# Kernel tuning notes

Measured on AMD Instinct MI355X. Metric: run time of the kernel, lower is better.

## Reference

```python
import jax, jax.numpy as jnp
import numpy as np

N_QUBITS = 10
N_LAYERS = 2
QSVT_DEGREE = 3
DT_RANK = 5  # n_qubits // 2
PI = np.float32(np.pi)

# ---- batched statevector simulation helpers (wire 0 = most significant, as in pennylane default.qubit) ----

def _apply_1q(s, wire, U):
    # s: (batch,) + (2,)*n complex; U: (batch,2,2) or (2,2)
    s = jnp.moveaxis(s, 1 + wire, 1)
    shp = s.shape
    s2 = s.reshape(shp[0], 2, -1)
    if U.ndim == 3:
        out = jnp.einsum('bij,bjr->bir', U, s2)
    else:
        out = jnp.einsum('ij,bjr->bir', U, s2)
    return jnp.moveaxis(out.reshape(shp), 1, 1 + wire)

def _ry(t):
    c = jnp.cos(t / 2).astype(jnp.complex64)
    s = jnp.sin(t / 2).astype(jnp.complex64)
    return jnp.stack([jnp.stack([c, -s], -1), jnp.stack([s, c], -1)], -2)

def _rz(t):
    e = jnp.exp(-0.5j * jnp.asarray(t).astype(jnp.complex64))
    z = jnp.zeros_like(e)
    return jnp.stack([jnp.stack([e, z], -1), jnp.stack([z, jnp.conj(e)], -1)], -2)

def _rx(t):
    c = jnp.cos(t / 2).astype(jnp.complex64)
    s = (-1j) * jnp.sin(t / 2).astype(jnp.complex64)
    return jnp.stack([jnp.stack([c, s], -1), jnp.stack([s, c], -1)], -2)

def _cnot(s, control, target):
    f = jnp.flip(s, axis=1 + target)
    s0 = jax.lax.index_in_dim(s, 0, axis=1 + control, keepdims=True)
    f1 = jax.lax.index_in_dim(f, 1, axis=1 + control, keepdims=True)
    return jnp.concatenate([s0, f1], axis=1 + control)

def _circuit(h, x, dt, cp, pc):
    """Batched selective QSVT circuit; h,x,dt: (B,n). Returns <Z_i> per wire, (B,n) float32."""
    n = N_QUBITS
    b = h.shape[0]
    s = jnp.zeros((b, 2 ** n), jnp.complex64).at[:, 0].set(1.0).reshape((b,) + (2,) * n)
    # 1. state encoding
    for i in range(n):
        s = _apply_1q(s, i, _ry(h[:, i]))
    # 2. delta-modulated QSVT block
    for d in range(QSVT_DEGREE + 1):
        for i in range(n):
            s = _apply_1q(s, i, _rz(pc[d] * dt[:, i] * PI))
        for i in range(n - 1):
            s = _cnot(s, i, i + 1)
        s = _cnot(s, n - 1, 0)
    # 3. variational block
    k = 0
    for _ in range(N_LAYERS):
        for i in range(n):
            s = _apply_1q(s, i, _rx(cp[k]))
            s = _apply_1q(s, i, _ry(cp[k + 1]))
            s = _apply_1q(s, i, _rz(cp[k + 2]))
            k += 3
        for i in range(n - 1):
            s = _cnot(s, i, i + 1)
    # 4. delta-modulated input encoding
    for i in range(n):
        s = _apply_1q(s, i, _ry(x[:, i] * dt[:, i]))
    # 5. <Z_i> measurements
    p = s.real ** 2 + s.imag ** 2
    zs = [(jax.lax.index_in_dim(p, 0, 1 + i, False) - jax.lax.index_in_dim(p, 1, 1 + i, False)).reshape(b, -1).sum(-1) for i in range(n)]
    return jnp.stack(zs, -1).astype(jnp.float32)

def setup_inputs() -> dict:
    key = jax.random.key(0)
    ks = jax.random.split(key, 6)
    B, S, n, r = 128, 512, N_QUBITS, DT_RANK
    angles = jax.random.uniform(ks[0], (B, S, n), jnp.float32) * PI  # angle encoding in [0, pi]
    W_x = jax.random.normal(ks[1], (r + 2 * n, n), jnp.float32) * 0.3  # x_proj weight (no bias)
    W_dt = jax.random.normal(ks[2], (n, r), jnp.float32) * 0.3  # dt_proj weight
    rng = np.random.default_rng(0)
    dt0 = np.exp(rng.random(n) * (np.log(0.1) - np.log(0.001)) + np.log(0.001))
    b_dt = jnp.asarray(dt0 + np.log(-np.expm1(-dt0)), jnp.float32)  # inverse-softplus init
    poly_coeffs = jax.random.normal(ks[3], (QSVT_DEGREE + 1,), jnp.float32) * 0.1
    circuit_params = jax.random.normal(ks[4], (n * N_LAYERS * 3,), jnp.float32) * 0.1
    D = jnp.ones((n,), jnp.float32)
    return {"angles": angles, "W_x": W_x, "W_dt": W_dt, "b_dt": b_dt,
            "poly_coeffs": poly_coeffs, "circuit_params": circuit_params, "D": D}

def reference(angles, W_x, W_dt, b_dt, poly_coeffs, circuit_params, D):
    # selective projections
    x_dbc = jnp.einsum('bsn,kn->bsk', angles, W_x)
    dt_raw = x_dbc[..., :DT_RANK]
    # B slice (x_dbc[..., DT_RANK:DT_RANK+n]) is computed but unused in the original forward
    C = x_dbc[..., DT_RANK + N_QUBITS:]
    dt = jax.nn.softplus(jnp.einsum('bsr,nr->bsn', dt_raw, W_dt) + b_dt)
    dt_angles = jnp.tanh(dt) * PI
    # quantum recurrence uses detached tensors in the original (torch .detach())
    x_sg = jax.lax.stop_gradient(angles)
    dt_sg = jax.lax.stop_gradient(dt_angles)
    cp = jax.lax.stop_gradient(circuit_params)
    pc = jax.lax.stop_gradient(poly_coeffs)

    def step(h, xs):
        x_t, d_t = xs
        h2 = _circuit(h, x_t, d_t, cp, pc)
        return h2, h2

    h0 = jnp.zeros((angles.shape[0], N_QUBITS), jnp.float32)
    _, hs = jax.lax.scan(step, h0, (jnp.swapaxes(x_sg, 0, 1), jnp.swapaxes(dt_sg, 0, 1)))
    hs = jnp.swapaxes(hs, 0, 1)  # (B,S,n)
    return C * hs + D * angles
```

## Files before the change

kernel.cpp:

```cpp
#include <hip/hip_runtime.h>
#include <math.h>


#define PIF 3.14159265358979323846f

constexpr int NQ = 10, SEQ = 512, NB = 128, NTHR = 512, RECF = 36;

struct CTbl { int mz[4][NQ]; };
constexpr CTbl build_tbl() {
  CTbl t{};
  unsigned mrow[NQ];
  for (int b = 0; b < NQ; ++b) mrow[b] = 1u << b;
  for (int d = 0; d < 4; ++d) {
    for (int i = 0; i < NQ; ++i) t.mz[d][i] = (int)mrow[9 - i];
    for (int i = 0; i < NQ - 1; ++i) { int bc = 9 - i, bt = 8 - i; mrow[bt] ^= mrow[bc]; }
    mrow[9] ^= mrow[0];
  }
  return t;
}
constexpr CTbl CT = build_tbl();

struct PermCols { int c4[10]; int cL[10]; };
constexpr PermCols build_perms() {
  PermCols P{};
  for (int b = 0; b < 10; ++b) {
    int x = 1 << b;
    for (int d = 0; d < 4; ++d) {
      for (int i = 0; i < 9; ++i) { int bc = 9 - i, bt = 8 - i; if ((x >> bc) & 1) x ^= (1 << bt); }
      if (x & 1) x ^= (1 << 9);
    }
    P.c4[b] = x;
    int y = 1 << b;
    for (int i = 0; i < 9; ++i) { int bc = 9 - i, bt = 8 - i; if ((y >> bc) & 1) y ^= (1 << bt); }
    P.cL[b] = y;
  }
  return P;
}
constexpr PermCols PC = build_perms();

constexpr int lanePart(int x)  { return ((x >> 0) & 1) | (((x >> 5) & 1) << 1) |
                                        (((x >> 1) & 1) << 2) | (((x >> 7) & 1) << 3) |
                                        (((x >> 3) & 1) << 4) | (((x >> 9) & 1) << 5); }
constexpr int wavePart8(int x) { return ((x >> 4) & 1) | (((x >> 8) & 1) << 1) |
                                        (((x >> 6) & 1) << 2); }

typedef __attribute__((ext_vector_type(2))) float v2;

constexpr int VOFS[8] = {0, 16, 256, 272, 64, 80, 320, 336};

template<int C>
__device__ __forceinline__ int dpp1(int x) {
  return __builtin_amdgcn_update_dpp(x, x, C, 0xF, 0xF, false);
}
template<int VL>
__device__ __forceinline__ int lxi(int x) {
  if constexpr (VL == 1)  return dpp1<0xB1>(x);
  else if constexpr (VL == 2)  return dpp1<0x4E>(x);
  else if constexpr (VL == 3)  return dpp1<0x1B>(x);
  else if constexpr (VL <= 7) {
    constexpr int q = (VL & 3) ^ 3;
    int y = x;
    if constexpr (q == 1) y = dpp1<0xB1>(y);
    else if constexpr (q == 2) y = dpp1<0x4E>(y);
    else if constexpr (q == 3) y = dpp1<0x1B>(y);
    return dpp1<0x141>(y);
  } else if constexpr (VL >= 12) {
    constexpr int q = (VL & 3) ^ 3;
    int y = x;
    if constexpr (q == 1) y = dpp1<0xB1>(y);
    else if constexpr (q == 2) y = dpp1<0x4E>(y);
    else if constexpr (q == 3) y = dpp1<0x1B>(y);
    return dpp1<0x140>(y);
  } else {
    constexpr int a = VL & 3;
    int y = x;
    if constexpr (a == 1) y = dpp1<0xB1>(y);
    else if constexpr (a == 2) y = dpp1<0x4E>(y);
    else if constexpr (a == 3) y = dpp1<0x1B>(y);
    y = dpp1<0x141>(y);
    return dpp1<0x140>(y);
  }
}
template<int VL>
__device__ __forceinline__ float lx(float x) {
  if constexpr (VL == 0) return x;
  else if constexpr (VL & 32) {
    int addr = (((int)threadIdx.x & 63) ^ VL) << 2;
    return __int_as_float(__builtin_amdgcn_ds_bpermute(addr, __float_as_int(x)));
  } else if constexpr (VL & 16) {
    return __int_as_float(__builtin_amdgcn_ds_swizzle(__float_as_int(x), (VL << 10) | 0x1F));
  } else {
    return __int_as_float(lxi<VL>(__float_as_int(x)));
  }
}
__device__ __forceinline__ float rdl(float x, int l) {
  return __int_as_float(__builtin_amdgcn_readlane(__float_as_int(x), l));
}

__device__ __forceinline__ int swz(int j) {
  return j ^ (((j >> 5) & 1) << 2) ^ ((j >> 7) & 1);
}

__device__ __forceinline__ void apply2(v2* amp, const v2* p, bool par, float4 U0, float4 U1) {
  v2 u00 = {U0.x, U0.y}, u01 = {U0.z, U0.w}, u10 = {U1.x, U1.y}, u11 = {U1.z, U1.w};
  v2 A = par ? u11 : u00, B = par ? u10 : u01;
  v2 An = {-A.y, A.y}, Bn = {-B.y, B.y};
#pragma unroll
  for (int r = 0; r < 2; ++r) {
    v2 o = amp[r], q = p[r];
    v2 res = A.x * o;
    res += An * __builtin_shufflevector(o, o, 1, 0);
    res += B.x * q;
    res += Bn * __builtin_shufflevector(q, q, 1, 0);
    amp[r] = res;
  }
}

template<int VL>
__device__ __forceinline__ void gate_lane2(v2* amp, float4 U0, float4 U1, int lane) {
  v2 p[2];
#pragma unroll
  for (int r = 0; r < 2; ++r) { p[r].x = lx<VL>(amp[r].x); p[r].y = lx<VL>(amp[r].y); }
  apply2(amp, p, (lane & VL) != 0, U0, U1);
}

__device__ __forceinline__ void gate_reg1(v2* amp, float4 U0, float4 U1) {
  v2 u00 = {U0.x, U0.y}, u01 = {U0.z, U0.w}, u10 = {U1.x, U1.y}, u11 = {U1.z, U1.w};
  v2 o0 = amp[0], o1 = amp[1];
  v2 a0 = {0.f, 0.f}, a1 = {0.f, 0.f};
  a0.x += u00.x * o0.x - u00.y * o0.y;  a0.y += u00.x * o0.y + u00.y * o0.x;
  a0.x += u01.x * o1.x - u01.y * o1.y;  a0.y += u01.x * o1.y + u01.y * o1.x;
  a1.x += u10.x * o0.x - u10.y * o0.y;  a1.y += u10.x * o0.y + u10.y * o0.x;
  a1.x += u11.x * o1.x - u11.y * o1.y;  a1.y += u11.x * o1.y + u11.y * o1.x;
  amp[0] = a0; amp[1] = a1;
}

template<int VL>
__device__ __forceinline__ float xdot_lane2(const v2* amp) {
  v2 acc = {0.f, 0.f};
#pragma unroll
  for (int r = 0; r < 2; ++r) {
    v2 p; p.x = lx<VL>(amp[r].x); p.y = lx<VL>(amp[r].y);
    acc += amp[r] * p;
  }
  return acc.x + acc.y;
}

__global__ __launch_bounds__(NTHR, 2) void qmamba_main(
    const float* __restrict__ angles, const float* __restrict__ Wx,
    const float* __restrict__ Wdt, const float* __restrict__ bdt,
    const float* __restrict__ pc, const float* __restrict__ cp,
    float* __restrict__ out)
{
  __shared__ float  tblL[SEQ][RECF];
  __shared__ float4 uuL[40];
  __shared__ v2     ex0[1024];
  __shared__ v2     ex1[1024];
  __shared__ float  zb[8][16];

  const int tid  = threadIdx.x;
  const int lane = tid & 63;
  const int wave = tid >> 6;
  const int b    = blockIdx.x;

  if (tid < 20) {
    int k = tid * 3;
    float al = 0.5f * cp[k], be = 0.5f * cp[k + 1], ga = 0.5f * cp[k + 2];
    float ca = __cosf(al), sa = __sinf(al);
    float cb = __cosf(be), sb = __sinf(be);
    float cg = __cosf(ga), sg = __sinf(ga);
    float2 M00 = make_float2(cb * ca,  sb * sa);
    float2 M01 = make_float2(-sb * ca, -cb * sa);
    float2 M10 = make_float2(sb * ca,  -cb * sa);
    float2 M11 = make_float2(cb * ca,  -sb * sa);
    float2 e0 = make_float2(cg, -sg), e1 = make_float2(cg, sg);
    auto cm = [](float2 a, float2 c) {
      return make_float2(a.x * c.x - a.y * c.y, a.x * c.y + a.y * c.x);
    };
    float2 u00 = cm(M00, e0), u01 = cm(M01, e0), u10 = cm(M10, e1), u11 = cm(M11, e1);
    uuL[2 * tid]     = make_float4(u00.x, u00.y, u01.x, u01.y);
    uuL[2 * tid + 1] = make_float4(u10.x, u10.y, u11.x, u11.y);
  }

  {
    const int t = tid;
    const float* ar = angles + (size_t)(b * SEQ + t) * NQ;
    float a[NQ];
#pragma unroll
    for (int n = 0; n < NQ; ++n) a[n] = ar[n];
    float dtr[5];
#pragma unroll
    for (int r = 0; r < 5; ++r) {
      float acc = 0.f;
#pragma unroll
      for (int n = 0; n < NQ; ++n) acc += a[n] * Wx[r * NQ + n];
      dtr[r] = acc;
    }
    float* rec = &tblL[t][0];
#pragma unroll
    for (int w = 0; w < NQ; ++w) {
      float lin = bdt[w];
#pragma unroll
      for (int r = 0; r < 5; ++r) lin += dtr[r] * Wdt[w * 5 + r];
      float sp = lin > 0.f ? lin + log1pf(__expf(-lin)) : log1pf(__expf(lin));
      float th = tanhf(sp) * PIF;
      float fa = a[w] * th;
      rec[w]      = th;
      rec[12 + w] = __cosf(fa);
      rec[24 + w] = __sinf(fa);
    }
  }
  __syncthreads();

  float pch[4];
#pragma unroll
  for (int d = 0; d < 4; ++d) pch[d] = 0.5f * pc[d] * PIF;

  v2 cw0[8], cw1[8];
  {
    const int s5 = wave & 1, s1 = (wave >> 1) & 1, s3 = (wave >> 2) & 1;
    auto ent = [&](int g, int row, int col) -> v2 {
      float4 R = uuL[2 * g + row];
      return col ? v2{R.z, R.w} : v2{R.x, R.y};
    };
    auto cmul = [](v2 a, v2 c) -> v2 {
      return v2{a.x * c.x - a.y * c.y, a.x * c.y + a.y * c.x};
    };
#pragma unroll
    for (int v = 0; v < 8; ++v) {
      const int v5 = v & 1, v1 = (v >> 1) & 1, v3 = (v >> 2) & 1;
      cw0[v] = cmul(cmul(ent(5,  s5, s5 ^ v5), ent(1,  s1, s1 ^ v1)), ent(3,  s3, s3 ^ v3));
      cw1[v] = cmul(cmul(ent(15, s5, s5 ^ v5), ent(11, s1, s1 ^ v1)), ent(13, s3, s3 ^ v3));
    }
  }

  unsigned PW0 = 0, PW1 = 0;
#pragma unroll
  for (int k = 0; k < 40; ++k) {
    const int m  = CT.mz[k / 10][k % 10];
    const int lm = lanePart(m), wm = wavePart8(m);
    unsigned flip = ((unsigned)((__popc(lane & lm) ^ __popc(wave & wm)) & 1)) ^ 1u;
    if (k < 32) PW0 |= flip << k; else PW1 |= flip << (k - 32);
  }

  int d4 = 0, dL = 0;
  if (lane & 1)  { d4 ^= PC.c4[0]; dL ^= PC.cL[0]; }
  if (lane & 2)  { d4 ^= PC.c4[5]; dL ^= PC.cL[5]; }
  if (lane & 4)  { d4 ^= PC.c4[1]; dL ^= PC.cL[1]; }
  if (lane & 8)  { d4 ^= PC.c4[7]; dL ^= PC.cL[7]; }
  if (lane & 16) { d4 ^= PC.c4[3]; dL ^= PC.cL[3]; }
  if (lane & 32) { d4 ^= PC.c4[9]; dL ^= PC.cL[9]; }
  if (wave & 1)  { d4 ^= PC.c4[4]; dL ^= PC.cL[4]; }
  if (wave & 2)  { d4 ^= PC.c4[8]; dL ^= PC.cL[8]; }
  if (wave & 4)  { d4 ^= PC.c4[6]; dL ^= PC.cL[6]; }
  const int oR4 = PC.c4[2], oRL = PC.cL[2];

  const int oidx = (lane & 1) | (((lane >> 1) & 1) << 5) | (((lane >> 2) & 1) << 1)
                 | (((lane >> 3) & 1) << 7) | (((lane >> 4) & 1) << 3) | (((lane >> 5) & 1) << 9)
                 | ((wave & 1) << 4) | (((wave >> 1) & 1) << 8) | (((wave >> 2) & 1) << 6);

  float hcw[NQ], hsw[NQ];
#pragma unroll
  for (int w = 0; w < NQ; ++w) { hcw[w] = 1.f; hsw[w] = 0.f; }

  v2 amp[2];

#pragma unroll 1
  for (int t = 0; t < SEQ; ++t) {
    float tha[12];
    {
      const float4* rq = (const float4*)&tblL[t][0];
#pragma unroll
      for (int j = 0; j < 3; ++j) ((float4*)tha)[j] = rq[j];
    }

    float F;
    F  = (lane & 1)  ? hsw[9] : hcw[9];
    F *= (lane & 2)  ? hsw[4] : hcw[4];
    F *= (lane & 4)  ? hsw[8] : hcw[8];
    F *= (lane & 8)  ? hsw[2] : hcw[2];
    F *= (lane & 16) ? hsw[6] : hcw[6];
    F *= (lane & 32) ? hsw[0] : hcw[0];
    F *= (wave & 1)  ? hsw[5] : hcw[5];
    F *= (wave & 2)  ? hsw[1] : hcw[1];
    F *= (wave & 4)  ? hsw[3] : hcw[3];
    const float G0 = F * hcw[7];
    const float G1 = F * hsw[7];

    float S0 = 0.f, S1 = 0.f;
#pragma unroll
    for (int k = 0; k < 40; ++k) {
      const int m  = CT.mz[k / 10][k % 10];
      float v = pch[k / 10] * tha[k % 10];
      unsigned fl = ((k < 32 ? (PW0 >> k) : (PW1 >> (k - 32))) & 1u) << 31;
      float sv = __int_as_float(__float_as_int(v) ^ fl);
      if ((m >> 2) & 1) S1 += sv; else S0 += sv;
    }
    {
      float sn, cs;
      __sincosf(S0 + S1, &sn, &cs); amp[0].x = G0 * cs; amp[0].y = G0 * sn;
      __sincosf(S0 - S1, &sn, &cs); amp[1].x = G1 * cs; amp[1].y = G1 * sn;
    }

    ex0[swz(d4)]       = amp[0];
    ex0[swz(d4 ^ oR4)] = amp[1];
    __syncthreads();
    {
      v2 pv0[8], pv1[8];
#pragma unroll
      for (int v = 0; v < 8; ++v) {
        const int base = oidx ^ VOFS[v];
        pv0[v] = ex0[swz(base)];
        pv1[v] = ex0[swz(base | 4)];
      }
      v2 a0 = {0.f, 0.f}, a1 = {0.f, 0.f};
#pragma unroll
      for (int v = 0; v < 8; ++v) {
        v2 c = cw0[v];
        a0.x += c.x * pv0[v].x - c.y * pv0[v].y;
        a0.y += c.x * pv0[v].y + c.y * pv0[v].x;
        a1.x += c.x * pv1[v].x - c.y * pv1[v].y;
        a1.y += c.x * pv1[v].y + c.y * pv1[v].x;
      }
      amp[0] = a0; amp[1] = a1;
    }
    gate_lane2<32>(amp, uuL[0],  uuL[1],  lane);
    gate_lane2<8> (amp, uuL[4],  uuL[5],  lane);
    gate_lane2<2> (amp, uuL[8],  uuL[9],  lane);
    gate_lane2<16>(amp, uuL[12], uuL[13], lane);
    gate_reg1     (amp, uuL[14], uuL[15]);
    gate_lane2<4> (amp, uuL[16], uuL[17], lane);
    gate_lane2<1> (amp, uuL[18], uuL[19], lane);

    ex1[swz(dL)]       = amp[0];
    ex1[swz(dL ^ oRL)] = amp[1];
    __syncthreads();
    {
      v2 pv0[8], pv1[8];
#pragma unroll
      for (int v = 0; v < 8; ++v) {
        const int base = oidx ^ VOFS[v];
        pv0[v] = ex1[swz(base)];
        pv1[v] = ex1[swz(base | 4)];
      }
      v2 a0 = {0.f, 0.f}, a1 = {0.f, 0.f};
#pragma unroll
      for (int v = 0; v < 8; ++v) {
        v2 c = cw1[v];
        a0.x += c.x * pv0[v].x - c.y * pv0[v].y;
        a0.y += c.x * pv0[v].y + c.y * pv0[v].x;
        a1.x += c.x * pv1[v].x - c.y * pv1[v].y;
        a1.y += c.x * pv1[v].y + c.y * pv1[v].x;
      }
      amp[0] = a0; amp[1] = a1;
    }
    gate_lane2<32>(amp, uuL[20], uuL[21], lane);
    gate_lane2<8> (amp, uuL[24], uuL[25], lane);
    gate_lane2<2> (amp, uuL[28], uuL[29], lane);
    gate_lane2<16>(amp, uuL[32], uuL[33], lane);
    gate_reg1     (amp, uuL[34], uuL[35]);
    gate_lane2<4> (amp, uuL[36], uuL[37], lane);
    gate_lane2<1> (amp, uuL[38], uuL[39], lane);

    ex0[swz(dL)]       = amp[0];
    ex0[swz(dL ^ oRL)] = amp[1];
    __syncthreads();
    v2 pw5[2], pw1[2], pw3[2];
    amp[0] = ex0[swz(oidx)];
    amp[1] = ex0[swz(oidx | 4)];
    pw5[0] = ex0[swz(oidx ^ 16)];   pw5[1] = ex0[swz((oidx ^ 16) | 4)];
    pw1[0] = ex0[swz(oidx ^ 256)];  pw1[1] = ex0[swz((oidx ^ 256) | 4)];
    pw3[0] = ex0[swz(oidx ^ 64)];   pw3[1] = ex0[swz((oidx ^ 64) | 4)];

    float cfv[12], sfv[12];
    {
      const float4* rq = (const float4*)&tblL[t][0];
#pragma unroll
      for (int j = 0; j < 3; ++j) { ((float4*)cfv)[j] = rq[3 + j]; ((float4*)sfv)[j] = rq[6 + j]; }
    }

    const float n0 = amp[0].x * amp[0].x + amp[0].y * amp[0].y;
    const float n1 = amp[1].x * amp[1].x + amp[1].y * amp[1].y;
    const float T0 = n0 + n1;
    const float T1 = n0 - n1;

    auto vdot2 = [](const v2* a, const v2* p) {
      v2 acc = a[0] * p[0] + a[1] * p[1];
      return acc.x + acc.y;
    };

    float zv[NQ];
    { float zp = (lane & 32) ? -T0 : T0; zv[0] = cfv[0] * zp - sfv[0] * xdot_lane2<32>(amp); }
    { float zp = (wave & 2)  ? -T0 : T0; zv[1] = cfv[1] * zp - sfv[1] * vdot2(amp, pw1); }
    { float zp = (lane & 8)  ? -T0 : T0; zv[2] = cfv[2] * zp - sfv[2] * xdot_lane2<8>(amp); }
    { float zp = (wave & 4)  ? -T0 : T0; zv[3] = cfv[3] * zp - sfv[3] * vdot2(amp, pw3); }
    { float zp = (lane & 2)  ? -T0 : T0; zv[4] = cfv[4] * zp - sfv[4] * xdot_lane2<2>(amp); }
    { float zp = (wave & 1)  ? -T0 : T0; zv[5] = cfv[5] * zp - sfv[5] * vdot2(amp, pw5); }
    { float zp = (lane & 16) ? -T0 : T0; zv[6] = cfv[6] * zp - sfv[6] * xdot_lane2<16>(amp); }
    { float xr = 2.f * (amp[0].x * amp[1].x + amp[0].y * amp[1].y);
      zv[7] = cfv[7] * T1 - sfv[7] * xr; }
    { float zp = (lane & 4)  ? -T0 : T0; zv[8] = cfv[8] * zp - sfv[8] * xdot_lane2<4>(amp); }
    { float zp = (lane & 1)  ? -T0 : T0; zv[9] = cfv[9] * zp - sfv[9] * xdot_lane2<1>(amp); }

#pragma unroll
    for (int w = 0; w < NQ; ++w) {
      zv[w] += lx<1>(zv[w]);
      zv[w] += lx<2>(zv[w]);
      zv[w] += lx<4>(zv[w]);
    }
    const int l7 = lane & 7;
    float c01 = (l7 & 1) ? zv[1] : zv[0];
    float c23 = (l7 & 1) ? zv[3] : zv[2];
    float c45 = (l7 & 1) ? zv[5] : zv[4];
    float c67 = (l7 & 1) ? zv[7] : zv[6];
    float c03 = (l7 & 2) ? c23 : c01;
    float c47 = (l7 & 2) ? c67 : c45;
    float pk  = (l7 & 4) ? c47 : c03;
    pk += lx<8>(pk);  pk += lx<16>(pk);  pk += lx<32>(pk);
    float z8 = zv[8]; z8 += lx<8>(z8); z8 += lx<16>(z8); z8 += lx<32>(z8);
    float z9 = zv[9]; z9 += lx<8>(z9); z9 += lx<16>(z9); z9 += lx<32>(z9);
    float zsel = pk;
    zsel = (lane == 8) ? z8 : zsel;
    zsel = (lane == 9) ? z9 : zsel;

    if (lane < NQ) zb[wave][lane] = zsel;
    __syncthreads();
    float z = 0.f;
    if (lane < NQ) {
      z = zb[0][lane] + zb[1][lane] + zb[2][lane] + zb[3][lane]
        + zb[4][lane] + zb[5][lane] + zb[6][lane] + zb[7][lane];
      if (wave == 0) out[(size_t)(b * SEQ + t) * NQ + lane] = z;
    }
    float sn_h, cs_h;
    __sincosf(0.5f * z, &sn_h, &cs_h);
#pragma unroll
    for (int w = 0; w < NQ; ++w) { hcw[w] = rdl(cs_h, w); hsw[w] = rdl(sn_h, w); }
  }
}

__global__ __launch_bounds__(256) void qmamba_post(
    const float* __restrict__ angles, const float* __restrict__ Wx,
    const float* __restrict__ Dg, float* __restrict__ out)
{
  int i = blockIdx.x * 256 + threadIdx.x;
  if (i >= NB * SEQ * NQ) return;
  int w  = i % NQ;
  int bt = i / NQ;
  const float* a = angles + (size_t)bt * NQ;
  float C = 0.f;
#pragma unroll
  for (int n = 0; n < NQ; ++n) C += a[n] * Wx[(15 + w) * NQ + n];
  float z = out[i];
  out[i] = C * z + Dg[w] * a[w];
}

extern "C" void kernel_launch(void* const* d_in, const int* in_sizes, int n_in,
                              void* d_out, int out_size, void* d_ws, size_t ws_size,
                              hipStream_t stream) {
  (void)in_sizes; (void)n_in; (void)out_size; (void)d_ws; (void)ws_size;
  const float* angles = (const float*)d_in[0];
  const float* Wx     = (const float*)d_in[1];
  const float* Wdt    = (const float*)d_in[2];
  const float* bdt    = (const float*)d_in[3];
  const float* pc     = (const float*)d_in[4];
  const float* cp     = (const float*)d_in[5];
  const float* Dg     = (const float*)d_in[6];
  float* out = (float*)d_out;
  hipLaunchKernelGGL(qmamba_main, dim3(NB), dim3(NTHR), 0, stream,
                     angles, Wx, Wdt, bdt, pc, cp, out);
  hipLaunchKernelGGL(qmamba_post, dim3((NB * SEQ * NQ + 255) / 256), dim3(256), 0, stream,
                     angles, Wx, Dg, out);
}
```

Baseline: 2.221 ms.

## Spread statevector over 16 waves with one amplitude per thread

Doubles the block to 1024 threads so each thread holds one amplitude instead of two. Qubit 2 moves from a register bit to a wave bit, so its mixing gate joins the LDS cross-wave exchange as a 16-term complex dot product. The mixing coefficients now live in shared memory instead of registers, and the per-thread phase sum is folded into precomputed per-qubit coefficients. Per-thread register pressure and serial work drop, at the cost of more waves per barrier, more LDS reads per exchange and fewer resident blocks per CU.

```diff
diff --git a/kernel.cpp b/kernel.cpp
--- a/kernel.cpp
+++ b/kernel.cpp
@@ -4,7 +4,7 @@
 
 #define PIF 3.14159265358979323846f
 
-constexpr int NQ = 10, SEQ = 512, NB = 128, NTHR = 512, RECF = 36;
+constexpr int NQ = 10, SEQ = 512, NB = 128, NTHR = 1024, RECF = 36;
 
 struct CTbl { int mz[4][NQ]; };
 constexpr CTbl build_tbl() {
@@ -38,15 +38,16 @@
 }
 constexpr PermCols PC = build_perms();
 
-constexpr int lanePart(int x)  { return ((x >> 0) & 1) | (((x >> 5) & 1) << 1) |
-                                        (((x >> 1) & 1) << 2) | (((x >> 7) & 1) << 3) |
-                                        (((x >> 3) & 1) << 4) | (((x >> 9) & 1) << 5); }
-constexpr int wavePart8(int x) { return ((x >> 4) & 1) | (((x >> 8) & 1) << 1) |
-                                        (((x >> 6) & 1) << 2); }
+constexpr int lanePart(int x)   { return ((x >> 0) & 1) | (((x >> 5) & 1) << 1) |
+                                         (((x >> 1) & 1) << 2) | (((x >> 7) & 1) << 3) |
+                                         (((x >> 3) & 1) << 4) | (((x >> 9) & 1) << 5); }
+constexpr int wavePart16(int x) { return ((x >> 4) & 1) | (((x >> 8) & 1) << 1) |
+                                         (((x >> 6) & 1) << 2) | (((x >> 2) & 1) << 3); }
 
 typedef __attribute__((ext_vector_type(2))) float v2;
 
-constexpr int VOFS[8] = {0, 16, 256, 272, 64, 80, 320, 336};
+constexpr int VOFS16[16] = {0, 16, 256, 272, 64, 80, 320, 336,
+                            4, 20, 260, 276, 68, 84, 324, 340};
 
 template<int C>
 __device__ __forceinline__ int dpp1(int x) {
@@ -97,56 +98,28 @@
   return __int_as_float(__builtin_amdgcn_readlane(__float_as_int(x), l));
 }
 
-__device__ __forceinline__ int swz(int j) {
-  return j ^ (((j >> 5) & 1) << 2) ^ ((j >> 7) & 1);
-}
-
-__device__ __forceinline__ void apply2(v2* amp, const v2* p, bool par, float4 U0, float4 U1) {
-  v2 u00 = {U0.x, U0.y}, u01 = {U0.z, U0.w}, u10 = {U1.x, U1.y}, u11 = {U1.z, U1.w};
-  v2 A = par ? u11 : u00, B = par ? u10 : u01;
-  v2 An = {-A.y, A.y}, Bn = {-B.y, B.y};
-#pragma unroll
-  for (int r = 0; r < 2; ++r) {
-    v2 o = amp[r], q = p[r];
-    v2 res = A.x * o;
-    res += An * __builtin_shufflevector(o, o, 1, 0);
-    res += B.x * q;
-    res += Bn * __builtin_shufflevector(q, q, 1, 0);
-    amp[r] = res;
-  }
-}
+__device__ __forceinline__ int swz16(int j) { return j ^ (((j >> 5) & 1) << 2); }
 
 template<int VL>
-__device__ __forceinline__ void gate_lane2(v2* amp, float4 U0, float4 U1, int lane) {
-  v2 p[2];
-#pragma unroll
-  for (int r = 0; r < 2; ++r) { p[r].x = lx<VL>(amp[r].x); p[r].y = lx<VL>(amp[r].y); }
-  apply2(amp, p, (lane & VL) != 0, U0, U1);
-}
-
-__device__ __forceinline__ void gate_reg1(v2* amp, float4 U0, float4 U1) {
-  v2 u00 = {U0.x, U0.y}, u01 = {U0.z, U0.w}, u10 = {U1.x, U1.y}, u11 = {U1.z, U1.w};
-  v2 o0 = amp[0], o1 = amp[1];
-  v2 a0 = {0.f, 0.f}, a1 = {0.f, 0.f};
-  a0.x += u00.x * o0.x - u00.y * o0.y;  a0.y += u00.x * o0.y + u00.y * o0.x;
-  a0.x += u01.x * o1.x - u01.y * o1.y;  a0.y += u01.x * o1.y + u01.y * o1.x;
-  a1.x += u10.x * o0.x - u10.y * o0.y;  a1.y += u10.x * o0.y + u10.y * o0.x;
-  a1.x += u11.x * o1.x - u11.y * o1.y;  a1.y += u11.x * o1.y + u11.y * o1.x;
-  amp[0] = a0; amp[1] = a1;
+__device__ __forceinline__ void gate1(v2& amp, float4 U0, float4 U1, int lane) {
+  float px = lx<VL>(amp.x), py = lx<VL>(amp.y);
+  const bool par = (lane & VL) != 0;
+  const float Ax = par ? U1.z : U0.x, Ay = par ? U1.w : U0.y;
+  const float Bx = par ? U1.x : U0.z, By = par ? U1.y : U0.w;
+  v2 res;
+  res.x = Ax * amp.x - Ay * amp.y + Bx * px - By * py;
+  res.y = Ax * amp.y + Ay * amp.x + Bx * py + By * px;
+  amp = res;
 }
 
 template<int VL>
-__device__ __forceinline__ float xdot_lane2(const v2* amp) {
-  v2 acc = {0.f, 0.f};
-#pragma unroll
-  for (int r = 0; r < 2; ++r) {
-    v2 p; p.x = lx<VL>(amp[r].x); p.y = lx<VL>(amp[r].y);
-    acc += amp[r] * p;
-  }
-  return acc.x + acc.y;
-}
-
-__global__ __launch_bounds__(NTHR, 2) void qmamba_main(
+__device__ __forceinline__ float xdot1(v2 amp) {
+  float px = lx<VL>(amp.x), py = lx<VL>(amp.y);
+  return amp.x * px + amp.y * py;
+}
+__device__ __forceinline__ float vdot1(v2 a, v2 p) { return a.x * p.x + a.y * p.y; }
+
+__global__ __launch_bounds__(NTHR, 4) void qmamba_main(
     const float* __restrict__ angles, const float* __restrict__ Wx,
     const float* __restrict__ Wdt, const float* __restrict__ bdt,
     const float* __restrict__ pc, const float* __restrict__ cp,
@@ -156,7 +129,8 @@
   __shared__ float4 uuL[40];
   __shared__ v2     ex0[1024];
   __shared__ v2     ex1[1024];
-  __shared__ float  zb[8][16];
+  __shared__ v2     cwT[2][16][16];
+  __shared__ float  zbT[16][16];
 
   const int tid  = threadIdx.x;
   const int lane = tid & 63;
@@ -183,7 +157,7 @@
   }
 
   {
-    const int t = tid;
+    const int t = tid >> 1, half = tid & 1;
     const float* ar = angles + (size_t)(b * SEQ + t) * NQ;
     float a[NQ];
 #pragma unroll
@@ -198,7 +172,8 @@
     }
     float* rec = &tblL[t][0];
 #pragma unroll
-    for (int w = 0; w < NQ; ++w) {
+    for (int ww = 0; ww < 5; ++ww) {
+      const int w = half * 5 + ww;
       float lin = bdt[w];
 #pragma unroll
       for (int r = 0; r < 5; ++r) lin += dtr[r] * Wdt[w * 5 + r];
@@ -212,13 +187,10 @@
   }
   __syncthreads();
 
-  float pch[4];
-#pragma unroll
-  for (int d = 0; d < 4; ++d) pch[d] = 0.5f * pc[d] * PIF;
-
-  v2 cw0[8], cw1[8];
-  {
-    const int s5 = wave & 1, s1 = (wave >> 1) & 1, s3 = (wave >> 2) & 1;
+  if (tid < 512) {
+    const int layer = tid >> 8, wv = (tid >> 4) & 15, v = tid & 15;
+    const int s5 = wv & 1, s1 = (wv >> 1) & 1, s3 = (wv >> 2) & 1, s7 = (wv >> 3) & 1;
+    const int v5 = v & 1, v1 = (v >> 1) & 1, v3 = (v >> 2) & 1, v7 = (v >> 3) & 1;
     auto ent = [&](int g, int row, int col) -> v2 {
       float4 R = uuL[2 * g + row];
       return col ? v2{R.z, R.w} : v2{R.x, R.y};
@@ -226,21 +198,29 @@
     auto cmul = [](v2 a, v2 c) -> v2 {
       return v2{a.x * c.x - a.y * c.y, a.x * c.y + a.y * c.x};
     };
-#pragma unroll
-    for (int v = 0; v < 8; ++v) {
-      const int v5 = v & 1, v1 = (v >> 1) & 1, v3 = (v >> 2) & 1;
-      cw0[v] = cmul(cmul(ent(5,  s5, s5 ^ v5), ent(1,  s1, s1 ^ v1)), ent(3,  s3, s3 ^ v3));
-      cw1[v] = cmul(cmul(ent(15, s5, s5 ^ v5), ent(11, s1, s1 ^ v1)), ent(13, s3, s3 ^ v3));
-    }
-  }
-
-  unsigned PW0 = 0, PW1 = 0;
-#pragma unroll
-  for (int k = 0; k < 40; ++k) {
-    const int m  = CT.mz[k / 10][k % 10];
-    const int lm = lanePart(m), wm = wavePart8(m);
-    unsigned flip = ((unsigned)((__popc(lane & lm) ^ __popc(wave & wm)) & 1)) ^ 1u;
-    if (k < 32) PW0 |= flip << k; else PW1 |= flip << (k - 32);
+    v2 c = ent(layer * 10 + 5, s5, s5 ^ v5);
+    c = cmul(c, ent(layer * 10 + 1, s1, s1 ^ v1));
+    c = cmul(c, ent(layer * 10 + 3, s3, s3 ^ v3));
+    c = cmul(c, ent(layer * 10 + 7, s7, s7 ^ v7));
+    cwT[layer][wv][v] = c;
+  }
+  __syncthreads();
+
+  float pch[4];
+#pragma unroll
+  for (int d = 0; d < 4; ++d) pch[d] = 0.5f * pc[d] * PIF;
+  float Ki[NQ];
+#pragma unroll
+  for (int i = 0; i < NQ; ++i) {
+    float k = 0.f;
+#pragma unroll
+    for (int d = 0; d < 4; ++d) {
+      const int m  = CT.mz[d][i];
+      const int lm = lanePart(m), wm = wavePart16(m);
+      const int par = (__popc(lane & lm) ^ __popc(wave & wm)) & 1;
+      k += par ? pch[d] : -pch[d];
+    }
+    Ki[i] = k;
   }
 
   int d4 = 0, dL = 0;
@@ -253,17 +233,23 @@
   if (wave & 1)  { d4 ^= PC.c4[4]; dL ^= PC.cL[4]; }
   if (wave & 2)  { d4 ^= PC.c4[8]; dL ^= PC.cL[8]; }
   if (wave & 4)  { d4 ^= PC.c4[6]; dL ^= PC.cL[6]; }
-  const int oR4 = PC.c4[2], oRL = PC.cL[2];
+  if (wave & 8)  { d4 ^= PC.c4[2]; dL ^= PC.cL[2]; }
 
   const int oidx = (lane & 1) | (((lane >> 1) & 1) << 5) | (((lane >> 2) & 1) << 1)
                  | (((lane >> 3) & 1) << 7) | (((lane >> 4) & 1) << 3) | (((lane >> 5) & 1) << 9)
-                 | ((wave & 1) << 4) | (((wave >> 1) & 1) << 8) | (((wave >> 2) & 1) << 6);
+                 | ((wave & 1) << 4) | (((wave >> 1) & 1) << 8)
+                 | (((wave >> 2) & 1) << 6) | (((wave >> 3) & 1) << 2);
+
+  const int w4 = swz16(d4), wL = swz16(dL);
+  int rofs[16];
+#pragma unroll
+  for (int v = 0; v < 16; ++v) rofs[v] = swz16(oidx ^ VOFS16[v]);
 
   float hcw[NQ], hsw[NQ];
 #pragma unroll
   for (int w = 0; w < NQ; ++w) { hcw[w] = 1.f; hsw[w] = 0.f; }
 
-  v2 amp[2];
+  v2 amp;
 
 #pragma unroll 1
   for (int t = 0; t < SEQ; ++t) {
@@ -284,93 +270,64 @@
     F *= (wave & 1)  ? hsw[5] : hcw[5];
     F *= (wave & 2)  ? hsw[1] : hcw[1];
     F *= (wave & 4)  ? hsw[3] : hcw[3];
-    const float G0 = F * hcw[7];
-    const float G1 = F * hsw[7];
-
-    float S0 = 0.f, S1 = 0.f;
-#pragma unroll
-    for (int k = 0; k < 40; ++k) {
-      const int m  = CT.mz[k / 10][k % 10];
-      float v = pch[k / 10] * tha[k % 10];
-      unsigned fl = ((k < 32 ? (PW0 >> k) : (PW1 >> (k - 32))) & 1u) << 31;
-      float sv = __int_as_float(__float_as_int(v) ^ fl);
-      if ((m >> 2) & 1) S1 += sv; else S0 += sv;
-    }
+    F *= (wave & 8)  ? hsw[7] : hcw[7];
+
+    float S = 0.f;
+#pragma unroll
+    for (int i = 0; i < NQ; ++i) S += Ki[i] * tha[i];
     {
       float sn, cs;
-      __sincosf(S0 + S1, &sn, &cs); amp[0].x = G0 * cs; amp[0].y = G0 * sn;
-      __sincosf(S0 - S1, &sn, &cs); amp[1].x = G1 * cs; amp[1].y = G1 * sn;
-    }
-
-    ex0[swz(d4)]       = amp[0];
-    ex0[swz(d4 ^ oR4)] = amp[1];
+      __sincosf(S, &sn, &cs);
+      amp.x = F * cs; amp.y = F * sn;
+    }
+
+    ex0[w4] = amp;
     __syncthreads();
     {
-      v2 pv0[8], pv1[8];
-#pragma unroll
-      for (int v = 0; v < 8; ++v) {
-        const int base = oidx ^ VOFS[v];
-        pv0[v] = ex0[swz(base)];
-        pv1[v] = ex0[swz(base | 4)];
+      v2 acc = {0.f, 0.f};
+#pragma unroll
+      for (int v = 0; v < 16; ++v) {
+        v2 p = ex0[rofs[v]];
+        v2 c = cwT[0][wave][v];
+        acc.x += c.x * p.x - c.y * p.y;
+        acc.y += c.x * p.y + c.y * p.x;
       }
-      v2 a0 = {0.f, 0.f}, a1 = {0.f, 0.f};
-#pragma unroll
-      for (int v = 0; v < 8; ++v) {
-        v2 c = cw0[v];
-        a0.x += c.x * pv0[v].x - c.y * pv0[v].y;
-        a0.y += c.x * pv0[v].y + c.y * pv0[v].x;
-        a1.x += c.x * pv1[v].x - c.y * pv1[v].y;
-        a1.y += c.x * pv1[v].y + c.y * pv1[v].x;
-      }
-      amp[0] = a0; amp[1] = a1;
-    }
-    gate_lane2<32>(amp, uuL[0],  uuL[1],  lane);
-    gate_lane2<8> (amp, uuL[4],  uuL[5],  lane);
-    gate_lane2<2> (amp, uuL[8],  uuL[9],  lane);
-    gate_lane2<16>(amp, uuL[12], uuL[13], lane);
-    gate_reg1     (amp, uuL[14], uuL[15]);
-    gate_lane2<4> (amp, uuL[16], uuL[17], lane);
-    gate_lane2<1> (amp, uuL[18], uuL[19], lane);
-
-    ex1[swz(dL)]       = amp[0];
-    ex1[swz(dL ^ oRL)] = amp[1];
+      amp = acc;
+    }
+    gate1<1> (amp, uuL[18], uuL[19], lane);
+    gate1<2> (amp, uuL[8],  uuL[9],  lane);
+    gate1<4> (amp, uuL[16], uuL[17], lane);
+    gate1<8> (amp, uuL[4],  uuL[5],  lane);
+    gate1<16>(amp, uuL[12], uuL[13], lane);
+    gate1<32>(amp, uuL[0],  uuL[1],  lane);
+
+    ex1[wL] = amp;
     __syncthreads();
     {
-      v2 pv0[8], pv1[8];
-#pragma unroll
-      for (int v = 0; v < 8; ++v) {
-        const int base = oidx ^ VOFS[v];
-        pv0[v] = ex1[swz(base)];
-        pv1[v] = ex1[swz(base | 4)];
+      v2 acc = {0.f, 0.f};
+#pragma unroll
+      for (int v = 0; v < 16; ++v) {
+        v2 p = ex1[rofs[v]];
+        v2 c = cwT[1][wave][v];
+        acc.x += c.x * p.x - c.y * p.y;
+        acc.y += c.x * p.y + c.y * p.x;
       }
-      v2 a0 = {0.f, 0.f}, a1 = {0.f, 0.f};
-#pragma unroll
-      for (int v = 0; v < 8; ++v) {
-        v2 c = cw1[v];
-        a0.x += c.x * pv0[v].x - c.y * pv0[v].y;
-        a0.y += c.x * pv0[v].y + c.y * pv0[v].x;
-        a1.x += c.x * pv1[v].x - c.y * pv1[v].y;
-        a1.y += c.x * pv1[v].y + c.y * pv1[v].x;
-      }
-      amp[0] = a0; amp[1] = a1;
-    }
-    gate_lane2<32>(amp, uuL[20], uuL[21], lane);
-    gate_lane2<8> (amp, uuL[24], uuL[25], lane);
-    gate_lane2<2> (amp, uuL[28], uuL[29], lane);
-    gate_lane2<16>(amp, uuL[32], uuL[33], lane);
-    gate_reg1     (amp, uuL[34], uuL[35]);
-    gate_lane2<4> (amp, uuL[36], uuL[37], lane);
-    gate_lane2<1> (amp, uuL[38], uuL[39], lane);
-
-    ex0[swz(dL)]       = amp[0];
-    ex0[swz(dL ^ oRL)] = amp[1];
+      amp = acc;
+    }
+    gate1<1> (amp, uuL[38], uuL[39], lane);
+    gate1<2> (amp, uuL[28], uuL[29], lane);
+    gate1<4> (amp, uuL[36], uuL[37], lane);
+    gate1<8> (amp, uuL[24], uuL[25], lane);
+    gate1<16>(amp, uuL[32], uuL[33], lane);
+    gate1<32>(amp, uuL[20], uuL[21], lane);
+
+    ex0[wL] = amp;
     __syncthreads();
-    v2 pw5[2], pw1[2], pw3[2];
-    amp[0] = ex0[swz(oidx)];
-    amp[1] = ex0[swz(oidx | 4)];
-    pw5[0] = ex0[swz(oidx ^ 16)];   pw5[1] = ex0[swz((oidx ^ 16) | 4)];
-    pw1[0] = ex0[swz(oidx ^ 256)];  pw1[1] = ex0[swz((oidx ^ 256) | 4)];
-    pw3[0] = ex0[swz(oidx ^ 64)];   pw3[1] = ex0[swz((oidx ^ 64) | 4)];
+    amp      = ex0[rofs[0]];
+    v2 p5    = ex0[rofs[1]];
+    v2 p1    = ex0[rofs[2]];
+    v2 p3    = ex0[rofs[4]];
+    v2 p7    = ex0[rofs[8]];
 
     float cfv[12], sfv[12];
     {
@@ -379,28 +336,19 @@
       for (int j = 0; j < 3; ++j) { ((float4*)cfv)[j] = rq[3 + j]; ((float4*)sfv)[j] = rq[6 + j]; }
     }
 
-    const float n0 = amp[0].x * amp[0].x + amp[0].y * amp[0].y;
-    const float n1 = amp[1].x * amp[1].x + amp[1].y * amp[1].y;
-    const float T0 = n0 + n1;
-    const float T1 = n0 - n1;
-
-    auto vdot2 = [](const v2* a, const v2* p) {
-      v2 acc = a[0] * p[0] + a[1] * p[1];
-      return acc.x + acc.y;
-    };
+    const float n = amp.x * amp.x + amp.y * amp.y;
 
     float zv[NQ];
-    { float zp = (lane & 32) ? -T0 : T0; zv[0] = cfv[0] * zp - sfv[0] * xdot_lane2<32>(amp); }
-    { float zp = (wave & 2)  ? -T0 : T0; zv[1] = cfv[1] * zp - sfv[1] * vdot2(amp, pw1); }
-    { float zp = (lane & 8)  ? -T0 : T0; zv[2] = cfv[2] * zp - sfv[2] * xdot_lane2<8>(amp); }
-    { float zp = (wave & 4)  ? -T0 : T0; zv[3] = cfv[3] * zp - sfv[3] * vdot2(amp, pw3); }
-    { float zp = (lane & 2)  ? -T0 : T0; zv[4] = cfv[4] * zp - sfv[4] * xdot_lane2<2>(amp); }
-    { float zp = (wave & 1)  ? -T0 : T0; zv[5] = cfv[5] * zp - sfv[5] * vdot2(amp, pw5); }
-    { float zp = (lane & 16) ? -T0 : T0; zv[6] = cfv[6] * zp - sfv[6] * xdot_lane2<16>(amp); }
-    { float xr = 2.f * (amp[0].x * amp[1].x + amp[0].y * amp[1].y);
-      zv[7] = cfv[7] * T1 - sfv[7] * xr; }
-    { float zp = (lane & 4)  ? -T0 : T0; zv[8] = cfv[8] * zp - sfv[8] * xdot_lane2<4>(amp); }
-    { float zp = (lane & 1)  ? -T0 : T0; zv[9] = cfv[9] * zp - sfv[9] * xdot_lane2<1>(amp); }
+    { float zp = (lane & 32) ? -n : n; zv[0] = cfv[0] * zp - sfv[0] * xdot1<32>(amp); }
+    { float zp = (wave & 2)  ? -n : n; zv[1] = cfv[1] * zp - sfv[1] * vdot1(amp, p1); }
+    { float zp = (lane & 8)  ? -n : n; zv[2] = cfv[2] * zp - sfv[2] * xdot1<8>(amp); }
+    { float zp = (wave & 4)  ? -n : n; zv[3] = cfv[3] * zp - sfv[3] * vdot1(amp, p3); }
+    { float zp = (lane & 2)  ? -n : n; zv[4] = cfv[4] * zp - sfv[4] * xdot1<2>(amp); }
+    { float zp = (wave & 1)  ? -n : n; zv[5] = cfv[5] * zp - sfv[5] * vdot1(amp, p5); }
+    { float zp = (lane & 16) ? -n : n; zv[6] = cfv[6] * zp - sfv[6] * xdot1<16>(amp); }
+    { float zp = (wave & 8)  ? -n : n; zv[7] = cfv[7] * zp - sfv[7] * vdot1(amp, p7); }
+    { float zp = (lane & 4)  ? -n : n; zv[8] = cfv[8] * zp - sfv[8] * xdot1<4>(amp); }
+    { float zp = (lane & 1)  ? -n : n; zv[9] = cfv[9] * zp - sfv[9] * xdot1<1>(amp); }
 
 #pragma unroll
     for (int w = 0; w < NQ; ++w) {
@@ -423,12 +371,14 @@
     zsel = (lane == 8) ? z8 : zsel;
     zsel = (lane == 9) ? z9 : zsel;
 
-    if (lane < NQ) zb[wave][lane] = zsel;
+    if (lane < NQ) zbT[lane][wave] = zsel;
     __syncthreads();
     float z = 0.f;
     if (lane < NQ) {
-      z = zb[0][lane] + zb[1][lane] + zb[2][lane] + zb[3][lane]
-        + zb[4][lane] + zb[5][lane] + zb[6][lane] + zb[7][lane];
+      const float4* zr = (const float4*)&zbT[lane][0];
+      float4 q0 = zr[0], q1 = zr[1], q2 = zr[2], q3 = zr[3];
+      z = ((q0.x + q0.y) + (q0.z + q0.w)) + ((q1.x + q1.y) + (q1.z + q1.w))
+        + ((q2.x + q2.y) + (q2.z + q2.w)) + ((q3.x + q3.y) + (q3.z + q3.w));
       if (wave == 0) out[(size_t)(b * SEQ + t) * NQ + lane] = z;
     }
     float sn_h, cs_h;
```

New measurement: 2.942 ms. 32.5% more time.
